# Performance work log

Hardware: AMD Instinct MI355X
Metric: run time of the kernel (lower is better)

The kernel has to match this reference:

```python
import jax, jax.numpy as jnp
import numpy as np

B, S, D, E, H = 1024, 256, 1024, 1024, 1024  # batch, state, belief, embedding, hidden
T1 = 32            # clip_length => number of scan steps
POSE_TILES = 4
MIN_STD = 0.1


def _gru(x, h, wih, whh, bih, bhh):
    # torch.nn.GRUCell semantics
    gi = x @ wih.T + bih
    gh = h @ whh.T + bhh
    i_r, i_z, i_n = jnp.split(gi, 3, axis=-1)
    h_r, h_z, h_n = jnp.split(gh, 3, axis=-1)
    r = jax.nn.sigmoid(i_r + h_r)
    z = jax.nn.sigmoid(i_z + h_z)
    n = jnp.tanh(i_n + r * h_n)
    return (1.0 - z) * n + z * h


def setup_inputs() -> dict:
    key = jax.random.key(0)
    ks = iter(jax.random.split(key, 40))
    g = lambda shape, s=1.0: jax.random.normal(next(ks), shape, dtype=jnp.float32) * s
    W = 0.02
    inp = {
        'prev_state': g((B, S)),
        'prev_belief': g((B, D)),
        'observations': g((T1, B, E)),
        'poses': g((T1, B, 6)),
        'noise_post': g((T1, B, S)),
        'noise_prior': g((T1, B, S)),
        # fc_embed_state_posterior: (2S+E) -> D
        'W_esq': g((D, 2 * S + E), W), 'b_esq': jnp.zeros((D,), jnp.float32),
        # fc_embed_state_prior: (2S+6*pose_tiles) -> D
        'W_esp': g((D, 2 * S + 6 * POSE_TILES), W), 'b_esp': jnp.zeros((D,), jnp.float32),
        # GRUCell posterior / prior
        'gq_wih': g((3 * D, D), W), 'gq_whh': g((3 * D, D), W),
        'gq_bih': jnp.zeros((3 * D,), jnp.float32), 'gq_bhh': jnp.zeros((3 * D,), jnp.float32),
        'gp_wih': g((3 * D, D), W), 'gp_whh': g((3 * D, D), W),
        'gp_bih': jnp.zeros((3 * D,), jnp.float32), 'gp_bhh': jnp.zeros((3 * D,), jnp.float32),
        # belief -> hidden -> 2*state heads
        'W_ebq': g((H, D), W), 'b_ebq': jnp.zeros((H,), jnp.float32),
        'W_sq': g((2 * S, H), W), 'b_sq': jnp.zeros((2 * S,), jnp.float32),
        'W_ebp': g((H, D), W), 'b_ebp': jnp.zeros((H,), jnp.float32),
        'W_sp': g((2 * S, H), W), 'b_sp': jnp.zeros((2 * S,), jnp.float32),
    }
    return inp


def reference(prev_state, prev_belief, observations, poses, noise_post, noise_prior,
              W_esq, b_esq, W_esp, b_esp,
              gq_wih, gq_whh, gq_bih, gq_bhh,
              gp_wih, gp_whh, gp_bih, gp_bhh,
              W_ebq, b_ebq, W_sq, b_sq, W_ebp, b_ebp, W_sp, b_sp):
    relu = jax.nn.relu

    def step(carry, xs):
        s_q, s_p, b_q, b_p = carry
        obs, pose, nq, npn = xs
        # posterior branch
        h = relu(jnp.concatenate([obs, s_q, s_p], axis=1) @ W_esq.T + b_esq)
        b_q_new = _gru(h, b_q, gq_wih, gq_whh, gq_bih, gq_bhh)
        hq = relu(b_q_new @ W_ebq.T + b_ebq)
        mq, raw_sq = jnp.split(hq @ W_sq.T + b_sq, 2, axis=1)
        std_q = jax.nn.softplus(raw_sq) + MIN_STD
        s_q_new = mq + std_q * nq
        # prior branch (uses old s_q, s_p per original code)
        pose_t = jnp.tile(pose, (1, POSE_TILES))
        h2 = relu(jnp.concatenate([pose_t, s_q, s_p], axis=1) @ W_esp.T + b_esp)
        b_p_new = _gru(h2, b_p, gp_wih, gp_whh, gp_bih, gp_bhh)
        hp = relu(b_p_new @ W_ebp.T + b_ebp)
        mp, raw_sp = jnp.split(hp @ W_sp.T + b_sp, 2, axis=1)
        std_p = jax.nn.softplus(raw_sp) + MIN_STD
        s_p_new = mp + std_p * npn
        new_carry = (s_q_new, s_p_new, b_q_new, b_p_new)
        ys = (b_q_new, s_p_new, mp, std_p, s_q_new, mq, std_q)
        return new_carry, ys

    carry0 = (prev_state, prev_state, prev_belief, prev_belief)
    _, ys = jax.lax.scan(step, carry0, (observations, poses, noise_post, noise_prior))
    post_beliefs, prior_states, prior_means, prior_stds, post_states, post_means, post_stds = ys
    # order matches torch: [posterior_beliefs, prior_states, prior_means, prior_std_devs,
    #                       posterior_states, posterior_means, posterior_std_devs]
    return (post_beliefs, prior_states, prior_means, prior_stds,
            post_states, post_means, post_stds)
```

## Files before the change

kernel.cpp:

```cpp
#include <hip/hip_runtime.h>
#include <stdint.h>
#include <math.h>

typedef unsigned short ushort_t;
typedef __attribute__((ext_vector_type(8))) short bf16x8;
typedef __attribute__((ext_vector_type(4))) float f32x4;

#define T1_ 32

__device__ __forceinline__ ushort_t f2bf(float f) {
  union { float f; unsigned int i; } v; v.f = f;
  unsigned int x = v.i;
  return (ushort_t)((x + 0x7FFFu + ((x >> 16) & 1u)) >> 16);
}
__device__ __forceinline__ float sigm(float x) { return 1.f / (1.f + expf(-x)); }

__device__ __forceinline__ void gld16(const ushort_t* g, ushort_t* l) {
  __builtin_amdgcn_global_load_lds(
      (const __attribute__((address_space(1))) unsigned int*)g,
      (__attribute__((address_space(3))) unsigned int*)l, 16, 0, 0);
}


__global__ __launch_bounds__(256) void cvt_k(const float* src, ushort_t* dst,
                                             long long n, int cols, int src_ld, int src_off) {
  const long long idx = (long long)blockIdx.x * 256 + threadIdx.x;
  if (idx >= n) return;
  const long long row = idx / cols;
  const int col = (int)(idx - row * cols);
  dst[idx] = f2bf(src[row * src_ld + src_off + col]);
}

__global__ __launch_bounds__(256) void wpe_k(const float* Wesp, float* wpe) {
  const int i = blockIdx.x * 256 + threadIdx.x;
  if (i >= 1024 * 6) return;
  const int n = i / 6, j = i % 6;
  float s = 0.f;
#pragma unroll
  for (int r = 0; r < 4; ++r) s += Wesp[(long long)n * 536 + j + 6 * r];
  wpe[i] = s;
}

__global__ void marker_k(float* out, float K) {
  if (threadIdx.x == 0 && blockIdx.x == 0) out[0] = K;
}

struct MMSide {
  const ushort_t* a0; const ushort_t* a1; const ushort_t* a2;
  int kd0, kd1, kd2;
  int coff0, coff1, coff2;
  const ushort_t* W; int ldw;
  const float* bias;
  ushort_t* outb;
  int dopose;
};
struct MM2Args { MMSide s[2]; const float* poses_t; const float* wpe; };

__global__ __launch_bounds__(256) void mm2_k(MM2Args g) {
  const MMSide S = g.s[blockIdx.z];
  __shared__ __align__(16) ushort_t As[2][1024];
  __shared__ __align__(16) ushort_t Ws[2][4096];
  const int tid = threadIdx.x;
  const int lane = tid & 63, wv = tid >> 6;
  const int wn = wv;
  const int bn0 = blockIdx.x * 128, bm0 = blockIdx.y * 32;
  const int srow = lane >> 2;
  const int sch8 = ((lane ^ (lane >> 2) ^ (lane >> 4)) & 3) * 8;
  const int rr = lane & 15, qq = lane >> 4;
  const int rslot8 = (((rr << 2) | ((qq ^ rr ^ (rr >> 2)) & 3)) * 8);

  f32x4 acc[2][2];
#pragma unroll
  for (int i = 0; i < 2; ++i)
#pragma unroll
    for (int j = 0; j < 2; ++j) acc[i][j] = (f32x4){0.f, 0.f, 0.f, 0.f};

  const int nk0 = S.kd0 >> 5, nk1 = S.kd1 >> 5, nk2 = S.kd2 >> 5;
  const int c1 = nk0, c2 = nk0 + nk1, nkt = c2 + nk2;

  auto stage = [&](int buf, int ktg) {
    const ushort_t* ab; int ktl, kdim, cf;
    if (ktg < c1)      { ab = S.a0; ktl = ktg;      kdim = S.kd0; cf = S.coff0; }
    else if (ktg < c2) { ab = S.a1; ktl = ktg - c1; kdim = S.kd1; cf = S.coff1; }
    else               { ab = S.a2; ktl = ktg - c2; kdim = S.kd2; cf = S.coff2; }
    const int k0 = ktl * 32;
    gld16(S.W + cf + (size_t)(bn0 + wv * 16 + srow) * S.ldw + k0 + sch8, &Ws[buf][wv * 512]);
    gld16(S.W + cf + (size_t)(bn0 + 64 + wv * 16 + srow) * S.ldw + k0 + sch8,
          &Ws[buf][(wv + 4) * 512]);
    if (wv < 2)
      gld16(ab + (size_t)(bm0 + wv * 16 + srow) * kdim + k0 + sch8, &As[buf][wv * 512]);
  };

  stage(0, 0);
  __syncthreads();
  int cur = 0;
#pragma unroll 1
  for (int ktg = 0; ktg < nkt; ++ktg) {
    if (ktg + 1 < nkt) stage(cur ^ 1, ktg + 1);
    bf16x8 a[2], b[2];
#pragma unroll
    for (int i = 0; i < 2; ++i)
      a[i] = *(const bf16x8*)&As[cur][i * 512 + rslot8];
#pragma unroll
    for (int j = 0; j < 2; ++j)
      b[j] = *(const bf16x8*)&Ws[cur][(wn * 2 + j) * 512 + rslot8];
#pragma unroll
    for (int i = 0; i < 2; ++i)
#pragma unroll
      for (int j = 0; j < 2; ++j)
        acc[i][j] = __builtin_amdgcn_mfma_f32_16x16x32_bf16(a[i], b[j], acc[i][j], 0, 0, 0);
    __syncthreads();
    cur ^= 1;
  }

  const int r15 = lane & 15, rq = (lane >> 4) * 4;
#pragma unroll
  for (int i = 0; i < 2; ++i) {
#pragma unroll
    for (int j = 0; j < 2; ++j) {
      const int col = bn0 + wn * 32 + j * 16 + r15;
      const float bs = S.bias[col];
#pragma unroll
      for (int q = 0; q < 4; ++q) {
        const int row = bm0 + i * 16 + rq + q;
        float v = acc[i][j][q] + bs;
        if (S.dopose) {
          float s = 0.f;
#pragma unroll
          for (int jj = 0; jj < 6; ++jj)
            s += g.poses_t[(long long)row * 6 + jj] * g.wpe[col * 6 + jj];
          v += s;
        }
        v = fmaxf(v, 0.f);
        S.outb[(size_t)row * 1024 + col] = f2bf(v);
      }
    }
  }
}

struct GruSide {
  const ushort_t* x;
  const ushort_t* hb;
  const float* hf;
  const ushort_t* wih; const ushort_t* whh;
  const float* bih; const float* bhh;
  float* dst; ushort_t* dstb;
};
struct Gru2Args { GruSide s[2]; };

__global__ __launch_bounds__(256) void gru2_k(Gru2Args g) {
  const GruSide S = g.s[blockIdx.z];
  __shared__ __align__(16) ushort_t lds[2][16384];
  const int tid = threadIdx.x;
  const int lane = tid & 63, wv = tid >> 6;
  const int wm = wv >> 1, wn = wv & 1;
  const int bn0 = blockIdx.x * 64, bm0 = blockIdx.y * 64;
  const int srow = lane >> 2;
  const int sch8 = ((lane ^ (lane >> 2) ^ (lane >> 4)) & 3) * 8;
  const int rr = lane & 15, qq = lane >> 4;
  const int rslot8 = (((rr << 2) | ((qq ^ rr ^ (rr >> 2)) & 3)) * 8);

  f32x4 aR[2][2], aZ[2][2], aNI[2][2], aNH[2][2];
#pragma unroll
  for (int i = 0; i < 2; ++i)
#pragma unroll
    for (int j = 0; j < 2; ++j) {
      aR[i][j] = (f32x4){0.f,0.f,0.f,0.f}; aZ[i][j] = (f32x4){0.f,0.f,0.f,0.f};
      aNI[i][j] = (f32x4){0.f,0.f,0.f,0.f}; aNH[i][j] = (f32x4){0.f,0.f,0.f,0.f};
    }

  auto stage = [&](int buf, int kt) {
    const int k0 = kt * 32;
#pragma unroll
    for (int u = 0; u < 8; ++u) {
      const int G = wv * 8 + u;
      if (G < 4)
        gld16(S.x + (size_t)(bm0 + G * 16 + srow) * 1024 + k0 + sch8, &lds[buf][G * 512]);
      else if (G < 8)
        gld16(S.hb + (size_t)(bm0 + (G - 4) * 16 + srow) * 1024 + k0 + sch8, &lds[buf][G * 512]);
      else {
        const int wch = G - 8, gg = wch >> 2, rc = wch & 3;
        const ushort_t* base = (gg < 3) ? S.wih : S.whh;
        const int gr = (gg < 3 ? gg : gg - 3) * 1024 + bn0 + rc * 16 + srow;
        gld16(base + (size_t)gr * 1024 + k0 + sch8, &lds[buf][G * 512]);
      }
    }
  };

  stage(0, 0);
  __syncthreads();
  int cur = 0;
#pragma unroll 1
  for (int kt = 0; kt < 32; ++kt) {
    if (kt + 1 < 32) stage(cur ^ 1, kt + 1);
    bf16x8 ax[2], ah[2], w[6][2];
#pragma unroll
    for (int i = 0; i < 2; ++i) {
      ax[i] = *(const bf16x8*)&lds[cur][(wm * 2 + i) * 512 + rslot8];
      ah[i] = *(const bf16x8*)&lds[cur][(4 + wm * 2 + i) * 512 + rslot8];
    }
#pragma unroll
    for (int gg = 0; gg < 6; ++gg)
#pragma unroll
      for (int j = 0; j < 2; ++j)
        w[gg][j] = *(const bf16x8*)&lds[cur][(8 + gg * 4 + wn * 2 + j) * 512 + rslot8];
#pragma unroll
    for (int i = 0; i < 2; ++i)
#pragma unroll
      for (int j = 0; j < 2; ++j) {
        aR[i][j]  = __builtin_amdgcn_mfma_f32_16x16x32_bf16(ax[i], w[0][j], aR[i][j], 0, 0, 0);
        aR[i][j]  = __builtin_amdgcn_mfma_f32_16x16x32_bf16(ah[i], w[3][j], aR[i][j], 0, 0, 0);
        aZ[i][j]  = __builtin_amdgcn_mfma_f32_16x16x32_bf16(ax[i], w[1][j], aZ[i][j], 0, 0, 0);
        aZ[i][j]  = __builtin_amdgcn_mfma_f32_16x16x32_bf16(ah[i], w[4][j], aZ[i][j], 0, 0, 0);
        aNI[i][j] = __builtin_amdgcn_mfma_f32_16x16x32_bf16(ax[i], w[2][j], aNI[i][j], 0, 0, 0);
        aNH[i][j] = __builtin_amdgcn_mfma_f32_16x16x32_bf16(ah[i], w[5][j], aNH[i][j], 0, 0, 0);
      }
    __syncthreads();
    cur ^= 1;
  }

  const int r15 = lane & 15, rq = (lane >> 4) * 4;
#pragma unroll
  for (int j = 0; j < 2; ++j) {
    const int col = bn0 + wn * 32 + j * 16 + r15;
    const float brz = S.bih[col] + S.bhh[col];
    const float bzz = S.bih[col + 1024] + S.bhh[col + 1024];
    const float bni = S.bih[col + 2048], bnh = S.bhh[col + 2048];
#pragma unroll
    for (int i = 0; i < 2; ++i) {
#pragma unroll
      for (int q = 0; q < 4; ++q) {
        const int row = bm0 + wm * 32 + i * 16 + rq + q;
        const float r = sigm(aR[i][j][q] + brz);
        const float z = sigm(aZ[i][j][q] + bzz);
        const float ng = tanhf(aNI[i][j][q] + bni + r * (aNH[i][j][q] + bnh));
        const size_t o = (size_t)row * 1024 + col;
        const float bnew = (1.f - z) * ng + z * S.hf[o];
        S.dst[o] = bnew;
        S.dstb[o] = f2bf(bnew);
      }
    }
  }
}

struct HeadSide {
  const ushort_t* hh;
  const ushort_t* Ws;
  const float* bs;
  const float* noise;
  float* omean; float* ostd; float* ostate;
  ushort_t* stateb;
};
struct Head2Args { HeadSide s[2]; };

__global__ __launch_bounds__(256) void head2_k(Head2Args g) {
  const HeadSide S = g.s[blockIdx.z];
  __shared__ __align__(16) ushort_t lds[2][3072];
  const int tid = threadIdx.x;
  const int lane = tid & 63, wv = tid >> 6;
  const int wm = wv >> 1, wn = wv & 1;
  const int bn0 = blockIdx.x * 32, bm0 = blockIdx.y * 32;
  const int srow = lane >> 2;
  const int sch8 = ((lane ^ (lane >> 2) ^ (lane >> 4)) & 3) * 8;
  const int rr = lane & 15, qq = lane >> 4;
  const int rslot8 = (((rr << 2) | ((qq ^ rr ^ (rr >> 2)) & 3)) * 8);

  f32x4 acc[2];
#pragma unroll
  for (int gg = 0; gg < 2; ++gg) acc[gg] = (f32x4){0.f, 0.f, 0.f, 0.f};

  auto stage = [&](int buf, int kt) {
    const int k0 = kt * 32;
    if (wv < 2) {
      gld16(S.hh + (size_t)(bm0 + wv * 16 + srow) * 1024 + k0 + sch8, &lds[buf][wv * 512]);
      gld16(S.Ws + (size_t)(bn0 + wv * 16 + srow) * 1024 + k0 + sch8, &lds[buf][(2 + wv) * 512]);
    } else {
      gld16(S.Ws + (size_t)(256 + bn0 + (wv - 2) * 16 + srow) * 1024 + k0 + sch8,
            &lds[buf][(2 + wv) * 512]);
    }
  };

  stage(0, 0);
  __syncthreads();
  int cur = 0;
#pragma unroll 1
  for (int kt = 0; kt < 32; ++kt) {
    if (kt + 1 < 32) stage(cur ^ 1, kt + 1);
    const bf16x8 a = *(const bf16x8*)&lds[cur][wm * 512 + rslot8];
    const bf16x8 w0 = *(const bf16x8*)&lds[cur][(2 + wn) * 512 + rslot8];
    const bf16x8 w1 = *(const bf16x8*)&lds[cur][(4 + wn) * 512 + rslot8];
    acc[0] = __builtin_amdgcn_mfma_f32_16x16x32_bf16(a, w0, acc[0], 0, 0, 0);
    acc[1] = __builtin_amdgcn_mfma_f32_16x16x32_bf16(a, w1, acc[1], 0, 0, 0);
    __syncthreads();
    cur ^= 1;
  }

  const int r15 = lane & 15, rq = (lane >> 4) * 4;
  const int col = bn0 + wn * 16 + r15;
  const float bm_ = S.bs[col];
  const float bsd = S.bs[col + 256];
#pragma unroll
  for (int q = 0; q < 4; ++q) {
    const int row = bm0 + wm * 16 + rq + q;
    const float mean = acc[0][q] + bm_;
    const float rs = acc[1][q] + bsd;
    const float sp = fmaxf(rs, 0.f) + log1pf(expf(-fabsf(rs)));
    const float sd = sp + 0.1f;
    const long long o = (long long)row * 256 + col;
    const float st = mean + sd * S.noise[o];
    S.omean[o] = mean; S.ostd[o] = sd; S.ostate[o] = st;
    S.stateb[o] = f2bf(st);
  }
}

extern "C" void kernel_launch(void* const* d_in, const int* in_sizes, int n_in,
                              void* d_out, int out_size, void* d_ws, size_t ws_size,
                              hipStream_t stream) {
  float* out = (float*)d_out;

  int gid = 0;
  if (n_in != 26) gid = 1;
  else if (out_size != 83886080) gid = 2;
  else if (in_sizes[0] != 262144 || in_sizes[1] != 1048576 || in_sizes[2] != 33554432 ||
           in_sizes[3] != 196608 || in_sizes[4] != 8388608 || in_sizes[5] != 8388608) gid = 3;
  else if (in_sizes[6] != 1572864 || in_sizes[8] != 548864) gid = 4;
  else if (in_sizes[10] != 3145728 || in_sizes[11] != 3145728 ||
           in_sizes[14] != 3145728 || in_sizes[15] != 3145728) gid = 5;
  else if (in_sizes[18] != 1048576 || in_sizes[20] != 524288 ||
           in_sizes[22] != 1048576 || in_sizes[24] != 524288) gid = 6;
  else if (ws_size < (128ull << 20)) gid = 7;
  if (gid != 0) {
    unsigned wsMB = (unsigned)(ws_size >> 20); if (wsMB > 4095u) wsMB = 4095u;
    const float K = (float)gid * 16777216.0f + (float)wsMB;
    hipLaunchKernelGGL(marker_k, dim3(1), dim3(64), 0, stream, out, K);
    return;
  }

  const float* prev_state  = (const float*)d_in[0];
  const float* prev_belief = (const float*)d_in[1];
  const float* observations= (const float*)d_in[2];
  const float* poses       = (const float*)d_in[3];
  const float* noise_post  = (const float*)d_in[4];
  const float* noise_prior = (const float*)d_in[5];
  const float* W_esq = (const float*)d_in[6];  const float* b_esq = (const float*)d_in[7];
  const float* W_esp = (const float*)d_in[8];  const float* b_esp = (const float*)d_in[9];
  const float* gq_wih = (const float*)d_in[10]; const float* gq_whh = (const float*)d_in[11];
  const float* gq_bih = (const float*)d_in[12]; const float* gq_bhh = (const float*)d_in[13];
  const float* gp_wih = (const float*)d_in[14]; const float* gp_whh = (const float*)d_in[15];
  const float* gp_bih = (const float*)d_in[16]; const float* gp_bhh = (const float*)d_in[17];
  const float* W_ebq = (const float*)d_in[18]; const float* b_ebq = (const float*)d_in[19];
  const float* W_sq  = (const float*)d_in[20]; const float* b_sq  = (const float*)d_in[21];
  const float* W_ebp = (const float*)d_in[22]; const float* b_ebp = (const float*)d_in[23];
  const float* W_sp  = (const float*)d_in[24]; const float* b_sp  = (const float*)d_in[25];

  float* out_belief = out;
  float* out_pstate = out + 33554432LL;
  float* out_pmean  = out + 41943040LL;
  float* out_pstd   = out + 50331648LL;
  float* out_qstate = out + 58720256LL;
  float* out_qmean  = out + 67108864LL;
  float* out_qstd   = out + 75497472LL;

  char* w = (char*)d_ws;
  ushort_t* obsb  = (ushort_t*)(w);
  ushort_t* wWesq = (ushort_t*)(w + (64ull << 20));
  ushort_t* wWesp = (ushort_t*)(w + (67ull << 20));
  ushort_t* wGqih = (ushort_t*)(w + (68ull << 20));
  ushort_t* wGqhh = (ushort_t*)(w + (74ull << 20));
  ushort_t* wGpih = (ushort_t*)(w + (80ull << 20));
  ushort_t* wGphh = (ushort_t*)(w + (86ull << 20));
  ushort_t* wEbq  = (ushort_t*)(w + (92ull << 20));
  ushort_t* wEbp  = (ushort_t*)(w + (94ull << 20));
  ushort_t* wSq   = (ushort_t*)(w + (96ull << 20));
  ushort_t* wSp   = (ushort_t*)(w + (97ull << 20));
  float*    wpe   = (float*)(w + (98ull << 20));
  ushort_t* h_q   = (ushort_t*)(w + (99ull << 20));
  ushort_t* h_p   = (ushort_t*)(w + (101ull << 20));
  ushort_t* bqb[2] = { (ushort_t*)(w + (103ull << 20)), (ushort_t*)(w + (105ull << 20)) };
  ushort_t* bpb[2] = { (ushort_t*)(w + (107ull << 20)), (ushort_t*)(w + (109ull << 20)) };
  ushort_t* sqb   = (ushort_t*)(w + (111ull << 20));
  ushort_t* spb   = (ushort_t*)(w + (111ull << 20) + 524288);
  float*    bpf[2] = { (float*)(w + (112ull << 20)), (float*)(w + (116ull << 20)) };

  const dim3 blk(256);
  auto cvt = [&](const float* s, ushort_t* d, long long n, int c, int ld, int off) {
    hipLaunchKernelGGL(cvt_k, dim3((unsigned)((n + 255) / 256)), blk, 0, stream, s, d, n, c, ld, off);
  };
  cvt(observations, obsb, 33554432LL, 1024, 1024, 0);
  cvt(W_esq, wWesq, 1572864LL, 1536, 1536, 0);
  cvt(W_esp, wWesp, 524288LL, 512, 536, 24);
  cvt(gq_wih, wGqih, 3145728LL, 1024, 1024, 0);
  cvt(gq_whh, wGqhh, 3145728LL, 1024, 1024, 0);
  cvt(gp_wih, wGpih, 3145728LL, 1024, 1024, 0);
  cvt(gp_whh, wGphh, 3145728LL, 1024, 1024, 0);
  cvt(W_ebq, wEbq, 1048576LL, 1024, 1024, 0);
  cvt(W_ebp, wEbp, 1048576LL, 1024, 1024, 0);
  cvt(W_sq, wSq, 524288LL, 1024, 1024, 0);
  cvt(W_sp, wSp, 524288LL, 1024, 1024, 0);
  cvt(prev_state, sqb, 262144LL, 256, 256, 0);
  cvt(prev_state, spb, 262144LL, 256, 256, 0);
  cvt(prev_belief, bqb[1], 1048576LL, 1024, 1024, 0);
  cvt(prev_belief, bpb[1], 1048576LL, 1024, 1024, 0);
  hipLaunchKernelGGL(wpe_k, dim3(24), blk, 0, stream, W_esp, wpe);

  for (int t = 0; t < T1_; ++t) {
    const int cur = t & 1, prv = cur ^ 1;
    const ushort_t* obs_t = obsb + (long long)t * 1048576;
    const float* bq_prev_f = (t == 0) ? prev_belief : out_belief + (long long)(t - 1) * 1048576;
    const float* bp_prev_f = (t == 0) ? prev_belief : bpf[prv];

    MM2Args a{};
    a.s[0] = MMSide{ obs_t, sqb, spb, 1024, 256, 256, 0, 1024, 1280,
                     wWesq, 1536, b_esq, h_q, 0 };
    a.s[1] = MMSide{ sqb, spb, nullptr, 256, 256, 0, 0, 256, 0,
                     wWesp, 512, b_esp, h_p, 1 };
    a.poses_t = poses + (long long)t * 6144; a.wpe = wpe;
    hipLaunchKernelGGL(mm2_k, dim3(8, 32, 2), blk, 0, stream, a);

    Gru2Args gr{};
    gr.s[0] = GruSide{ h_q, bqb[prv], bq_prev_f, wGqih, wGqhh, gq_bih, gq_bhh,
                       out_belief + (long long)t * 1048576, bqb[cur] };
    gr.s[1] = GruSide{ h_p, bpb[prv], bp_prev_f, wGpih, wGphh, gp_bih, gp_bhh,
                       bpf[cur], bpb[cur] };
    hipLaunchKernelGGL(gru2_k, dim3(16, 16, 2), blk, 0, stream, gr);

    a = MM2Args{};
    a.s[0] = MMSide{ bqb[cur], nullptr, nullptr, 1024, 0, 0, 0, 0, 0,
                     wEbq, 1024, b_ebq, h_q, 0 };
    a.s[1] = MMSide{ bpb[cur], nullptr, nullptr, 1024, 0, 0, 0, 0, 0,
                     wEbp, 1024, b_ebp, h_p, 0 };
    hipLaunchKernelGGL(mm2_k, dim3(8, 32, 2), blk, 0, stream, a);

    Head2Args hd{};
    hd.s[0] = HeadSide{ h_q, wSq, b_sq, noise_post + (long long)t * 262144,
                        out_qmean + (long long)t * 262144,
                        out_qstd + (long long)t * 262144,
                        out_qstate + (long long)t * 262144, sqb };
    hd.s[1] = HeadSide{ h_p, wSp, b_sp, noise_prior + (long long)t * 262144,
                        out_pmean + (long long)t * 262144,
                        out_pstd + (long long)t * 262144,
                        out_pstate + (long long)t * 262144, spb };
    hipLaunchKernelGGL(head2_k, dim3(8, 32, 2), blk, 0, stream, hd);
  }
}
```

Measured before the change: 3.585 ms.

## Precompute observation projection for all timesteps in one batched GEMM

Moves the observation part of the posterior embedding (obs @ W_esq[:, :1024]^T) out of the sequential scan into a single large GEMM over all 32 timesteps before the loop. The per-step mm2 kernel now only handles the 512-wide state columns and adds the precomputed bf16 partial sum in its epilogue. This cuts the per-step K dimension for the posterior side from 1536 to 512 and balances it with the prior side. In exchange it needs 64MB more workspace, adds a bf16 rounding of the partial sum, and adds an extra read per output element.

Result: faster. 3.465 ms (median of 2 runs) (-3.4%).

```diff
diff --git a/kernel.cpp b/kernel.cpp
--- a/kernel.cpp
+++ b/kernel.cpp
@@ -8,6 +8,9 @@
 
 #define T1_ 32
 
+__device__ __forceinline__ float bf2f(ushort_t u) {
+  union { unsigned int i; float f; } v; v.i = ((unsigned int)u) << 16; return v.f;
+}
 __device__ __forceinline__ ushort_t f2bf(float f) {
   union { float f; unsigned int i; } v; v.f = f;
   unsigned int x = v.i;
@@ -43,6 +46,69 @@
 
 __global__ void marker_k(float* out, float K) {
   if (threadIdx.x == 0 && blockIdx.x == 0) out[0] = K;
+}
+
+struct ObsqArgs { const ushort_t* A; const ushort_t* W; ushort_t* out; };
+__global__ __launch_bounds__(256) void obsq_k(ObsqArgs g) {
+  __shared__ __align__(16) ushort_t As[2][2048];
+  __shared__ __align__(16) ushort_t Ws[2][4096];
+  const int tid = threadIdx.x;
+  const int lane = tid & 63, wv = tid >> 6;
+  const int wm = wv >> 1, wn = wv & 1;
+  const int bn0 = blockIdx.x * 128, bm0 = blockIdx.y * 64;
+  const int srow = lane >> 2;
+  const int sch8 = ((lane ^ (lane >> 2) ^ (lane >> 4)) & 3) * 8;
+  const int rr = lane & 15, qq = lane >> 4;
+  const int rslot8 = (((rr << 2) | ((qq ^ rr ^ (rr >> 2)) & 3)) * 8);
+
+  f32x4 acc[2][4];
+#pragma unroll
+  for (int i = 0; i < 2; ++i)
+#pragma unroll
+    for (int j = 0; j < 4; ++j) acc[i][j] = (f32x4){0.f, 0.f, 0.f, 0.f};
+
+  auto stage = [&](int buf, int kt) {
+    const int k0 = kt * 32;
+    gld16(g.A + (size_t)(bm0 + wv * 16 + srow) * 1024 + k0 + sch8, &As[buf][wv * 512]);
+    gld16(g.W + (size_t)(bn0 + wv * 16 + srow) * 1536 + k0 + sch8, &Ws[buf][wv * 512]);
+    gld16(g.W + (size_t)(bn0 + 64 + wv * 16 + srow) * 1536 + k0 + sch8,
+          &Ws[buf][2048 + wv * 512]);
+  };
+
+  stage(0, 0);
+  __syncthreads();
+  int cur = 0;
+#pragma unroll 1
+  for (int kt = 0; kt < 32; ++kt) {
+    if (kt + 1 < 32) stage(cur ^ 1, kt + 1);
+    bf16x8 a[2], b[4];
+#pragma unroll
+    for (int i = 0; i < 2; ++i)
+      a[i] = *(const bf16x8*)&As[cur][(wm * 2 + i) * 512 + rslot8];
+#pragma unroll
+    for (int j = 0; j < 4; ++j)
+      b[j] = *(const bf16x8*)&Ws[cur][(wn * 4 + j) * 512 + rslot8];
+#pragma unroll
+    for (int i = 0; i < 2; ++i)
+#pragma unroll
+      for (int j = 0; j < 4; ++j)
+        acc[i][j] = __builtin_amdgcn_mfma_f32_16x16x32_bf16(a[i], b[j], acc[i][j], 0, 0, 0);
+    __syncthreads();
+    cur ^= 1;
+  }
+
+  const int r15 = lane & 15, rq = (lane >> 4) * 4;
+#pragma unroll
+  for (int i = 0; i < 2; ++i)
+#pragma unroll
+    for (int j = 0; j < 4; ++j) {
+      const int col = bn0 + wn * 64 + j * 16 + r15;
+#pragma unroll
+      for (int q = 0; q < 4; ++q) {
+        const int row = bm0 + wm * 32 + i * 16 + rq + q;
+        g.out[(size_t)row * 1024 + col] = f2bf(acc[i][j][q]);
+      }
+    }
 }
 
 struct MMSide {
@@ -53,6 +119,7 @@
   const float* bias;
   ushort_t* outb;
   int dopose;
+  const ushort_t* extrab;
 };
 struct MM2Args { MMSide s[2]; const float* poses_t; const float* wpe; };
 
@@ -124,6 +191,7 @@
       for (int q = 0; q < 4; ++q) {
         const int row = bm0 + i * 16 + rq + q;
         float v = acc[i][j][q] + bs;
+        if (S.extrab) v += bf2f(S.extrab[(size_t)row * 1024 + col]);
         if (S.dopose) {
           float s = 0.f;
 #pragma unroll
@@ -328,7 +396,7 @@
            in_sizes[14] != 3145728 || in_sizes[15] != 3145728) gid = 5;
   else if (in_sizes[18] != 1048576 || in_sizes[20] != 524288 ||
            in_sizes[22] != 1048576 || in_sizes[24] != 524288) gid = 6;
-  else if (ws_size < (128ull << 20)) gid = 7;
+  else if (ws_size < (184ull << 20)) gid = 7;
   if (gid != 0) {
     unsigned wsMB = (unsigned)(ws_size >> 20); if (wsMB > 4095u) wsMB = 4095u;
     const float K = (float)gid * 16777216.0f + (float)wsMB;
@@ -363,24 +431,25 @@
 
   char* w = (char*)d_ws;
   ushort_t* obsb  = (ushort_t*)(w);
-  ushort_t* wWesq = (ushort_t*)(w + (64ull << 20));
-  ushort_t* wWesp = (ushort_t*)(w + (67ull << 20));
-  ushort_t* wGqih = (ushort_t*)(w + (68ull << 20));
-  ushort_t* wGqhh = (ushort_t*)(w + (74ull << 20));
-  ushort_t* wGpih = (ushort_t*)(w + (80ull << 20));
-  ushort_t* wGphh = (ushort_t*)(w + (86ull << 20));
-  ushort_t* wEbq  = (ushort_t*)(w + (92ull << 20));
-  ushort_t* wEbp  = (ushort_t*)(w + (94ull << 20));
-  ushort_t* wSq   = (ushort_t*)(w + (96ull << 20));
-  ushort_t* wSp   = (ushort_t*)(w + (97ull << 20));
-  float*    wpe   = (float*)(w + (98ull << 20));
-  ushort_t* h_q   = (ushort_t*)(w + (99ull << 20));
-  ushort_t* h_p   = (ushort_t*)(w + (101ull << 20));
-  ushort_t* bqb[2] = { (ushort_t*)(w + (103ull << 20)), (ushort_t*)(w + (105ull << 20)) };
-  ushort_t* bpb[2] = { (ushort_t*)(w + (107ull << 20)), (ushort_t*)(w + (109ull << 20)) };
-  ushort_t* sqb   = (ushort_t*)(w + (111ull << 20));
-  ushort_t* spb   = (ushort_t*)(w + (111ull << 20) + 524288);
-  float*    bpf[2] = { (float*)(w + (112ull << 20)), (float*)(w + (116ull << 20)) };
+  ushort_t* OBSQ  = (ushort_t*)(w + (64ull << 20));
+  ushort_t* wWesq = (ushort_t*)(w + (128ull << 20));
+  ushort_t* wWesp = (ushort_t*)(w + (131ull << 20));
+  ushort_t* wGqih = (ushort_t*)(w + (132ull << 20));
+  ushort_t* wGqhh = (ushort_t*)(w + (138ull << 20));
+  ushort_t* wGpih = (ushort_t*)(w + (144ull << 20));
+  ushort_t* wGphh = (ushort_t*)(w + (150ull << 20));
+  ushort_t* wEbq  = (ushort_t*)(w + (156ull << 20));
+  ushort_t* wEbp  = (ushort_t*)(w + (158ull << 20));
+  ushort_t* wSq   = (ushort_t*)(w + (160ull << 20));
+  ushort_t* wSp   = (ushort_t*)(w + (161ull << 20));
+  float*    wpe   = (float*)(w + (162ull << 20));
+  ushort_t* h_q   = (ushort_t*)(w + (163ull << 20));
+  ushort_t* h_p   = (ushort_t*)(w + (165ull << 20));
+  ushort_t* bqb[2] = { (ushort_t*)(w + (167ull << 20)), (ushort_t*)(w + (169ull << 20)) };
+  ushort_t* bpb[2] = { (ushort_t*)(w + (171ull << 20)), (ushort_t*)(w + (173ull << 20)) };
+  ushort_t* sqb   = (ushort_t*)(w + (175ull << 20));
+  ushort_t* spb   = (ushort_t*)(w + (175ull << 20) + 524288);
+  float*    bpf[2] = { (float*)(w + (176ull << 20)), (float*)(w + (180ull << 20)) };
 
   const dim3 blk(256);
   auto cvt = [&](const float* s, ushort_t* d, long long n, int c, int ld, int off) {
@@ -403,17 +472,21 @@
   cvt(prev_belief, bpb[1], 1048576LL, 1024, 1024, 0);
   hipLaunchKernelGGL(wpe_k, dim3(24), blk, 0, stream, W_esp, wpe);
 
+  {
+    ObsqArgs oa{ obsb, wWesq, OBSQ };
+    hipLaunchKernelGGL(obsq_k, dim3(8, 512), blk, 0, stream, oa);
+  }
+
   for (int t = 0; t < T1_; ++t) {
     const int cur = t & 1, prv = cur ^ 1;
-    const ushort_t* obs_t = obsb + (long long)t * 1048576;
     const float* bq_prev_f = (t == 0) ? prev_belief : out_belief + (long long)(t - 1) * 1048576;
     const float* bp_prev_f = (t == 0) ? prev_belief : bpf[prv];
 
     MM2Args a{};
-    a.s[0] = MMSide{ obs_t, sqb, spb, 1024, 256, 256, 0, 1024, 1280,
-                     wWesq, 1536, b_esq, h_q, 0 };
+    a.s[0] = MMSide{ sqb, spb, nullptr, 256, 256, 0, 1024, 1280, 0,
+                     wWesq, 1536, b_esq, h_q, 0, OBSQ + (long long)t * 1048576 };
     a.s[1] = MMSide{ sqb, spb, nullptr, 256, 256, 0, 0, 256, 0,
-                     wWesp, 512, b_esp, h_p, 1 };
+                     wWesp, 512, b_esp, h_p, 1, nullptr };
     a.poses_t = poses + (long long)t * 6144; a.wpe = wpe;
     hipLaunchKernelGGL(mm2_k, dim3(8, 32, 2), blk, 0, stream, a);
 
@@ -426,9 +499,9 @@
 
     a = MM2Args{};
     a.s[0] = MMSide{ bqb[cur], nullptr, nullptr, 1024, 0, 0, 0, 0, 0,
-                     wEbq, 1024, b_ebq, h_q, 0 };
+                     wEbq, 1024, b_ebq, h_q, 0, nullptr };
     a.s[1] = MMSide{ bpb[cur], nullptr, nullptr, 1024, 0, 0, 0, 0, 0,
-                     wEbp, 1024, b_ebp, h_p, 0 };
+                     wEbp, 1024, b_ebp, h_p, 0, nullptr };
     hipLaunchKernelGGL(mm2_k, dim3(8, 32, 2), blk, 0, stream, a);
 
     Head2Args hd{};
```
